# Performance work log

Hardware: AMD Instinct MI355X
Metric: run time of the kernel (lower is better)

## Reference

```python
import jax, jax.numpy as jnp
import numpy as np

N, E, DIN, ED, H, C = 50000, 800000, 128, 16, 4, 128
HC = H * C
SLOPE = 0.2


def gat_conv(x, ei_src, ei_dst, ea, W, a_src, a_dst, We, a_e, b):
    # x: [N, din]; ea: [E, ed] (self-loops already appended by caller)
    n = x.shape[0]
    h = (x @ W).reshape(n, H, C)                       # [N,H,C]
    al_src = (h * a_src).sum(-1)                       # [N,H]
    al_dst = (h * a_dst).sum(-1)                       # [N,H]
    e = (ea @ We).reshape(-1, H, C)                    # [E,H,C]
    al_e = (e * a_e).sum(-1)                           # [E,H]
    alpha = al_src[ei_src] + al_dst[ei_dst] + al_e     # [E,H]
    alpha = jnp.where(alpha > 0, alpha, SLOPE * alpha)  # LeakyReLU(0.2)
    # per-destination-node segment softmax (stable)
    amax = jax.ops.segment_max(alpha, ei_dst, num_segments=n)
    amax = jnp.where(jnp.isfinite(amax), amax, 0.0)
    ex = jnp.exp(alpha - amax[ei_dst])
    den = jax.ops.segment_sum(ex, ei_dst, num_segments=n)
    alpha = ex / (den[ei_dst] + 1e-16)                 # [E,H]
    msg = h[ei_src] * alpha[:, :, None]                # [E,H,C]
    out = jax.ops.segment_sum(msg, ei_dst, num_segments=n)  # [N,H,C]
    return out.reshape(n, HC) + b


def setup_inputs() -> dict:
    key = jax.random.key(0)
    ks = jax.random.split(key, 16)
    s = 0.05
    inp = {
        "x": jax.random.normal(ks[0], (N, DIN), jnp.float32),
        "edge_index": jax.random.randint(ks[1], (2, E), 0, N, jnp.int64),
        "edge_features": jax.random.normal(ks[2], (E, ED), jnp.float32),
        # layer 1 params
        "W1": jax.random.normal(ks[3], (DIN, HC), jnp.float32) * s,
        "att_src1": jax.random.normal(ks[4], (H, C), jnp.float32) * s,
        "att_dst1": jax.random.normal(ks[5], (H, C), jnp.float32) * s,
        "lin_e1": jax.random.normal(ks[6], (ED, HC), jnp.float32) * s,
        "att_e1": jax.random.normal(ks[7], (H, C), jnp.float32) * s,
        "b1": jnp.zeros((HC,), jnp.float32),
        # layer 2 params
        "W2": jax.random.normal(ks[8], (HC, HC), jnp.float32) * s,
        "att_src2": jax.random.normal(ks[9], (H, C), jnp.float32) * s,
        "att_dst2": jax.random.normal(ks[10], (H, C), jnp.float32) * s,
        "lin_e2": jax.random.normal(ks[11], (ED, HC), jnp.float32) * s,
        "att_e2": jax.random.normal(ks[12], (H, C), jnp.float32) * s,
        "b2": jnp.zeros((HC,), jnp.float32),
    }
    return inp


def reference(x, edge_index, edge_features,
              W1, att_src1, att_dst1, lin_e1, att_e1, b1,
              W2, att_src2, att_dst2, lin_e2, att_e2, b2):
    # add self-loops once (PyG default: add_self_loops=True, edge_attr fill='mean')
    loop = jnp.arange(N, dtype=edge_index.dtype)
    ei_src = jnp.concatenate([edge_index[0], loop])
    ei_dst = jnp.concatenate([edge_index[1], loop])
    mean_ea = edge_features.mean(0)
    ea = jnp.concatenate([edge_features, jnp.broadcast_to(mean_ea, (N, ED))], axis=0)

    h = gat_conv(x, ei_src, ei_dst, ea, W1, att_src1, att_dst1, lin_e1, att_e1, b1)
    h = jax.nn.elu(h)
    h = gat_conv(h, ei_src, ei_dst, ea, W2, att_src2, att_dst2, lin_e2, att_e2, b2)
    return jax.nn.elu(h)
```

## Files before the change

kernel.cpp:

```cpp
#include <hip/hip_runtime.h>
#include <math.h>

#define NNODE 50000
#define NEDGE 800000
#define DINv  128
#define EDv   16
#define NHv   4
#define CHv   128
#define HCv   512
#define SLOPEv 0.2f
#define MEANBLK 512
#define CONVN (NNODE * DINv / 4)

typedef __attribute__((ext_vector_type(8))) short bf16x8;
typedef __attribute__((ext_vector_type(4))) float f32x4;
typedef __attribute__((ext_vector_type(4))) unsigned u32x4;
typedef __attribute__((address_space(3))) unsigned lds_u32;
typedef const __attribute__((address_space(1))) unsigned glb_u32;

__device__ __forceinline__ ushort f2b(float f) {
  unsigned u = __float_as_uint(f);
  u += 0x7FFF + ((u >> 16) & 1);
  return (ushort)(u >> 16);
}
__device__ __forceinline__ float blo(unsigned u) { return __uint_as_float(u << 16); }
__device__ __forceinline__ float bhi(unsigned u) { return __uint_as_float(u & 0xffff0000u); }

__device__ __forceinline__ void nt_store16(void* p, unsigned a, unsigned b, unsigned c,
                                           unsigned d) {
  u32x4 t = {a, b, c, d};
  __builtin_nontemporal_store(t, (u32x4*)p);
}

__global__ void detect_kernel(const int* __restrict__ ei, int* __restrict__ flag) {
  __shared__ int bad;
  if (threadIdx.x == 0) bad = 0;
  __syncthreads();
  for (int i = threadIdx.x; i < 2048; i += 256)
    if (ei[2 * i + 1] != 0) bad = 1;
  __syncthreads();
  if (threadIdx.x == 0) flag[0] = bad ? 0 : 1;
}

__device__ __forceinline__ int load_idx(const int* __restrict__ ei, int e, int row, int wide) {
  if (wide) return ei[2 * ((size_t)row * NEDGE + e)];
  return ei[(size_t)row * NEDGE + e];
}

__global__ void count_kernel(const int* __restrict__ ei, const int* __restrict__ flag,
                             int* __restrict__ deg) {
  int e = blockIdx.x * blockDim.x + threadIdx.x;
  if (e < NEDGE) {
    int w = flag[0];
    atomicAdd(&deg[load_idx(ei, e, 1, w)], 1);
  }
}

__global__ void scatter_kernel(const int* __restrict__ ei, const int* __restrict__ flag,
                               const int* __restrict__ row_ptr, int* __restrict__ cursor,
                               int* __restrict__ eid_sorted) {
  int e = blockIdx.x * blockDim.x + threadIdx.x;
  if (e < NEDGE) {
    int w = flag[0];
    int d = load_idx(ei, e, 1, w);
    int p = row_ptr[d] + atomicAdd(&cursor[d], 1);
    eid_sorted[p] = e;
  }
}

__global__ void prep_misc_kernel(const float* __restrict__ ea, float* __restrict__ partials,
                                 const float* __restrict__ We1, const float* __restrict__ ae1,
                                 const float* __restrict__ We2, const float* __restrict__ ae2,
                                 float* __restrict__ v1, float* __restrict__ v2,
                                 const float* __restrict__ x, const float* __restrict__ W1,
                                 const float* __restrict__ W2, ushort* __restrict__ xb,
                                 ushort* __restrict__ Bt1, ushort* __restrict__ Bt2) {
  int b = blockIdx.x;
  if (b < MEANBLK) {
    float acc[EDv];
#pragma unroll
    for (int d = 0; d < EDv; d++) acc[d] = 0.f;
    const int stride = MEANBLK * 256;
    for (int r = b * 256 + threadIdx.x; r < NEDGE; r += stride) {
      const float4* p = (const float4*)(ea + (size_t)r * EDv);
#pragma unroll
      for (int q = 0; q < 4; q++) {
        float4 v = p[q];
        acc[q * 4 + 0] += v.x; acc[q * 4 + 1] += v.y;
        acc[q * 4 + 2] += v.z; acc[q * 4 + 3] += v.w;
      }
    }
    __shared__ float red[4][EDv];
    int wid = threadIdx.x >> 6, lane = threadIdx.x & 63;
#pragma unroll
    for (int d = 0; d < EDv; d++) {
      float v = acc[d];
      for (int off = 32; off; off >>= 1) v += __shfl_down(v, off, 64);
      if (lane == 0) red[wid][d] = v;
    }
    __syncthreads();
    if (threadIdx.x < EDv) {
      float v = red[0][threadIdx.x] + red[1][threadIdx.x] + red[2][threadIdx.x] +
                red[3][threadIdx.x];
      partials[b * EDv + threadIdx.x] = v;
    }
  } else if (b == MEANBLK) {
    int t = threadIdx.x;
    if (t < 128) {
      int layer = t >> 6, u = t & 63;
      int d = u >> 2, h = u & 3;
      const float* We = layer ? We2 : We1;
      const float* ae = layer ? ae2 : ae1;
      float s = 0.f;
      for (int c = 0; c < CHv; c++) s += We[(size_t)d * HCv + h * CHv + c] * ae[h * CHv + c];
      (layer ? v2 : v1)[d * 4 + h] = s;
    }
  } else {
    int i = (b - MEANBLK - 1) * 256 + threadIdx.x;
    if (i < CONVN) {
      float4 v = ((const float4*)x)[i];
      ushort4 o;
      o.x = f2b(v.x); o.y = f2b(v.y); o.z = f2b(v.z); o.w = f2b(v.w);
      ((ushort4*)xb)[i] = o;
    } else if (i < CONVN + DINv * HCv) {
      int idx = i - CONVN;
      int k = idx >> 9, n = idx & (HCv - 1);
      Bt1[(size_t)n * DINv + k] = f2b(W1[idx]);
    } else if (i < CONVN + DINv * HCv + HCv * HCv) {
      int idx = i - CONVN - DINv * HCv;
      int k = idx >> 9, n = idx & (HCv - 1);
      Bt2[(size_t)n * HCv + k] = f2b(W2[idx]);
    }
  }
}

__global__ __launch_bounds__(1024) void scan_fold_kernel(
    const int* __restrict__ deg, int* __restrict__ row_ptr,
    const float* __restrict__ partials, const float* __restrict__ v1,
    const float* __restrict__ v2, float* __restrict__ loop1, float* __restrict__ loop2) {
  int tid = threadIdx.x;
  if (blockIdx.x == 0) {
    __shared__ int wsum[16];
    int wid = tid >> 6, lane = tid & 63;
    int carry = 0;
    for (int base = 0; base < NNODE; base += 4096) {
      int idx = base + tid * 4;
      int4 x = make_int4(0, 0, 0, 0);
      if (idx < NNODE) x = *(const int4*)(deg + idx);
      int t0 = x.x, t1 = t0 + x.y, t2 = t1 + x.z, t3 = t2 + x.w;
      int v = t3;
#pragma unroll
      for (int off = 1; off < 64; off <<= 1) {
        int t = __shfl_up(v, off, 64);
        if (lane >= off) v += t;
      }
      if (lane == 63) wsum[wid] = v;
      __syncthreads();
      if (wid == 0) {
        int s = (lane < 16) ? wsum[lane] : 0;
#pragma unroll
        for (int off = 1; off < 16; off <<= 1) {
          int t = __shfl_up(s, off, 64);
          if (lane >= off) s += t;
        }
        if (lane < 16) wsum[lane] = s;
      }
      __syncthreads();
      int woff = wid ? wsum[wid - 1] : 0;
      int excl = carry + woff + v - t3;
      if (idx < NNODE) {
        int4 o = make_int4(excl, excl + t0, excl + t1, excl + t2);
        *(int4*)(row_ptr + idx) = o;
      }
      carry += wsum[15];
      __syncthreads();
    }
    if (tid == 0) row_ptr[NNODE] = carry;
  } else {
    __shared__ float buf[1024];
    __shared__ float ms[16];
    int d = tid & 15, r0 = tid >> 4;
    float v = 0.f;
    for (int r = r0; r < MEANBLK; r += 64) v += partials[r * EDv + d];
    buf[tid] = v;
    __syncthreads();
#pragma unroll
    for (int off = 32; off >= 1; off >>= 1) {
      if (r0 < off) buf[tid] += buf[tid + off * 16];
      __syncthreads();
    }
    if (tid < 16) ms[tid] = buf[tid] * (1.0f / NEDGE);
    __syncthreads();
    if (tid < 8) {
      const float* vv = (tid >> 2) ? v2 : v1;
      int h = tid & 3;
      float a = 0.f;
      for (int d2 = 0; d2 < EDv; d2++) a += ms[d2] * vv[d2 * 4 + h];
      ((tid >> 2) ? loop2 : loop1)[h] = a;
    }
  }
}

__global__ void apre1_kernel(const int* __restrict__ eid_sorted, const int* __restrict__ ei,
                             const int* __restrict__ flag,
                             const float* __restrict__ ea, const float* __restrict__ al_src,
                             const float* __restrict__ v1, const float* __restrict__ v2,
                             float* __restrict__ ap1, float* __restrict__ ale2s,
                             int* __restrict__ src_sorted) {
  __shared__ float sv1[64], sv2[64];
  if (threadIdx.x < 64) sv1[threadIdx.x] = v1[threadIdx.x];
  else if (threadIdx.x < 128) sv2[threadIdx.x - 64] = v2[threadIdx.x - 64];
  __syncthreads();
  int p = blockIdx.x * 256 + threadIdx.x;
  if (p >= NEDGE) return;
  int e = eid_sorted[p];
  int w = flag[0];
  int s = load_idx(ei, e, 0, w);
  const float4* pr = (const float4*)(ea + (size_t)e * EDv);
  float row[16];
  *(float4*)&row[0] = pr[0]; *(float4*)&row[4] = pr[1];
  *(float4*)&row[8] = pr[2]; *(float4*)&row[12] = pr[3];
  float a0 = 0, a1 = 0, a2 = 0, a3 = 0;
  float b0 = 0, b1 = 0, b2 = 0, b3 = 0;
#pragma unroll
  for (int d = 0; d < 16; d++) {
    a0 += row[d] * sv1[d * 4 + 0];
    a1 += row[d] * sv1[d * 4 + 1];
    a2 += row[d] * sv1[d * 4 + 2];
    a3 += row[d] * sv1[d * 4 + 3];
    b0 += row[d] * sv2[d * 4 + 0];
    b1 += row[d] * sv2[d * 4 + 1];
    b2 += row[d] * sv2[d * 4 + 2];
    b3 += row[d] * sv2[d * 4 + 3];
  }
  float4 as = ((const float4*)al_src)[s];
  ((float4*)ap1)[p] = make_float4(as.x + a0, as.y + a1, as.z + a2, as.w + a3);
  ((float4*)ale2s)[p] = make_float4(b0, b1, b2, b3);
  src_sorted[p] = s;
}

__global__ void apre2_kernel(const int* __restrict__ src_sorted, const float* __restrict__ ale2s,
                             const float* __restrict__ al_src, float* __restrict__ ap2) {
  int p = blockIdx.x * 256 + threadIdx.x;
  if (p >= NEDGE) return;
  int s = src_sorted[p];
  float4 a = ((const float4*)al_src)[s];
  float4 b = ((const float4*)ale2s)[p];
  ((float4*)ap2)[p] = make_float4(a.x + b.x, a.y + b.y, a.z + b.z, a.w + b.w);
}

__global__ __launch_bounds__(256) void gemm_mfma_kernel(const ushort* __restrict__ A,
                                                        const ushort* __restrict__ Bt,
                                                        ushort* __restrict__ C, int M, int K,
                                                        const float* __restrict__ a_src,
                                                        const float* __restrict__ a_dst,
                                                        float* __restrict__ al_src,
                                                        float* __restrict__ al_dst) {
  __shared__ ushort As[8][128][8];
  __shared__ ushort Bs[8][128][8];
  __shared__ float ssa[128], ssd[128];
  __shared__ float rsum[2][128][2];
  int tid = threadIdx.x;
  int wid = tid >> 6, lane = tid & 63;

  int nblk = gridDim.x * gridDim.y;
  int j = blockIdx.y * gridDim.x + blockIdx.x;
  int q = nblk >> 3, rem = nblk & 7;
  int xcd = j & 7, idx = j >> 3;
  int d = (xcd < rem) ? xcd * (q + 1) + idx : rem * (q + 1) + (xcd - rem) * q + idx;
  int rb = (d >> 2) * 128, cb = (d & 3) * 128;
  int hblk = cb >> 7;

  int wm = (wid >> 1) * 64, wn = (wid & 1) * 64;
  int lr = lane & 15, lq = lane >> 4;

  if (tid < 128) { ssa[tid] = a_src[cb + tid]; ssd[tid] = a_dst[cb + tid]; }

  f32x4 acc[4][4];
#pragma unroll
  for (int i = 0; i < 4; i++)
#pragma unroll
    for (int jx = 0; jx < 4; jx++) acc[i][jx] = (f32x4){0.f, 0.f, 0.f, 0.f};

  ushort* AsF = &As[0][0][0];
  ushort* BsF = &Bs[0][0][0];

  for (int k0 = 0; k0 < K; k0 += 64) {
#pragma unroll
    for (int s = 0; s < 4; s++) {
      int c = s * 256 + tid;
      int kq = c >> 7, m = c & 127;
      int row = rb + m; if (row >= M) row = M - 1;
      const ushort* gA = A + (size_t)row * K + k0 + kq * 8;
      __builtin_amdgcn_global_load_lds((glb_u32*)gA, (lds_u32*)(AsF + (size_t)c * 8), 16, 0, 0);
    }
#pragma unroll
    for (int s = 0; s < 4; s++) {
      int c = s * 256 + tid;
      int kq = c >> 7, n = c & 127;
      const ushort* gB = Bt + (size_t)(cb + n) * K + k0 + kq * 8;
      __builtin_amdgcn_global_load_lds((glb_u32*)gB, (lds_u32*)(BsF + (size_t)c * 8), 16, 0, 0);
    }
    __syncthreads();
#pragma unroll
    for (int hh = 0; hh < 2; hh++) {
      bf16x8 af[4], bfr[4];
#pragma unroll
      for (int i = 0; i < 4; i++) {
        af[i]  = *(const bf16x8*)&As[hh * 4 + lq][wm + i * 16 + lr][0];
        bfr[i] = *(const bf16x8*)&Bs[hh * 4 + lq][wn + i * 16 + lr][0];
      }
#pragma unroll
      for (int i = 0; i < 4; i++)
#pragma unroll
        for (int jx = 0; jx < 4; jx++)
          acc[i][jx] = __builtin_amdgcn_mfma_f32_16x16x32_bf16(af[i], bfr[jx], acc[i][jx], 0, 0, 0);
    }
    __syncthreads();
  }

#pragma unroll
  for (int i = 0; i < 4; i++) {
    int rbase = rb + wm + i * 16 + lq * 4;
#pragma unroll
    for (int jx = 0; jx < 4; jx++) {
      int col = cb + wn + jx * 16 + lr;
#pragma unroll
      for (int r = 0; r < 4; r++) {
        int row = rbase + r;
        if (row < M) C[(size_t)row * HCv + col] = f2b(acc[i][jx][r]);
      }
    }
  }

  float sa[4], sd[4];
#pragma unroll
  for (int jx = 0; jx < 4; jx++) {
    int c = wn + jx * 16 + lr;
    sa[jx] = ssa[c]; sd[jx] = ssd[c];
  }
#pragma unroll
  for (int i = 0; i < 4; i++) {
#pragma unroll
    for (int r = 0; r < 4; r++) {
      float s1 = 0.f, s2 = 0.f;
#pragma unroll
      for (int jx = 0; jx < 4; jx++) {
        s1 = fmaf(acc[i][jx][r], sa[jx], s1);
        s2 = fmaf(acc[i][jx][r], sd[jx], s2);
      }
#pragma unroll
      for (int off = 1; off < 16; off <<= 1) {
        s1 += __shfl_xor(s1, off, 16);
        s2 += __shfl_xor(s2, off, 16);
      }
      if (lr == 0) {
        int row = wm + i * 16 + lq * 4 + r;
        rsum[0][row][wn >> 6] = s1;
        rsum[1][row][wn >> 6] = s2;
      }
    }
  }
  __syncthreads();
  if (tid < 128) {
    int row = rb + tid;
    if (row < M) {
      al_src[(size_t)row * 4 + hblk] = rsum[0][tid][0] + rsum[0][tid][1];
      al_dst[(size_t)row * 4 + hblk] = rsum[1][tid][0] + rsum[1][tid][1];
    }
  }
}

__device__ __forceinline__ void fma8(float* acc, float w, uint4 u) {
  acc[0] = fmaf(w, blo(u.x), acc[0]);
  acc[1] = fmaf(w, bhi(u.x), acc[1]);
  acc[2] = fmaf(w, blo(u.y), acc[2]);
  acc[3] = fmaf(w, bhi(u.y), acc[3]);
  acc[4] = fmaf(w, blo(u.z), acc[4]);
  acc[5] = fmaf(w, bhi(u.z), acc[5]);
  acc[6] = fmaf(w, blo(u.w), acc[6]);
  acc[7] = fmaf(w, bhi(u.w), acc[7]);
}

__global__ __launch_bounds__(256) void node_kernel(
    const ushort* __restrict__ hb, const float* __restrict__ al_src,
    const float* __restrict__ al_dst, const float* __restrict__ ap,
    const float* __restrict__ loop_al_e, const int* __restrict__ row_ptr,
    const int* __restrict__ src_sorted, const float* __restrict__ bias,
    float* __restrict__ outf, ushort* __restrict__ outb) {
  int wid = threadIdx.x >> 6, lane = threadIdx.x & 63;
  int n = blockIdx.x * 4 + wid;
  if (n >= NNODE) return;
  int base = row_ptr[n];
  int deg = row_ptr[n + 1] - base;
  int h = lane >> 4;
  int jj = lane & 15;

  float aldh = al_dst[(size_t)n * 4 + h];
  float a0 = al_src[(size_t)n * 4 + h] + aldh + loop_al_e[h];
  float alph = a0 > 0.f ? a0 : SLOPEv * a0;
  float wl = __expf(alph);

  uint4 uself = *((const uint4*)(hb + ((size_t)n << 9)) + lane);

  float acc[8];
#pragma unroll
  for (int q = 0; q < 8; q++) acc[q] = 0.f;
  float den = 0.f;

  for (int cs = 0; cs < deg; cs += 16) {
    int cl = min(16, deg - cs);
    float w = 0.f;
    int sv = 0;
    if (jj < cl) {
      int p = base + cs + jj;
      sv = src_sorted[p];
      float a = ap[(size_t)p * 4 + h] + aldh;
      a = a > 0.f ? a : SLOPEv * a;
      w = __expf(a);
      den += w;
    }
    int cl4 = (cl + 3) & ~3;
    for (int j0 = 0; j0 < cl4; j0 += 4) {
      int s0 = __shfl(sv, j0 + 0, 16);
      int s1 = __shfl(sv, j0 + 1, 16);
      int s2 = __shfl(sv, j0 + 2, 16);
      int s3 = __shfl(sv, j0 + 3, 16);
      float w0 = __shfl(w, j0 + 0, 16);
      float w1 = __shfl(w, j0 + 1, 16);
      float w2 = __shfl(w, j0 + 2, 16);
      float w3 = __shfl(w, j0 + 3, 16);
      uint4 u0 = *((const uint4*)(hb + ((size_t)s0 << 9)) + lane);
      uint4 u1 = *((const uint4*)(hb + ((size_t)s1 << 9)) + lane);
      uint4 u2 = *((const uint4*)(hb + ((size_t)s2 << 9)) + lane);
      uint4 u3 = *((const uint4*)(hb + ((size_t)s3 << 9)) + lane);
      fma8(acc, w0, u0);
      fma8(acc, w1, u1);
      fma8(acc, w2, u2);
      fma8(acc, w3, u3);
    }
  }

  fma8(acc, wl, uself);

#pragma unroll
  for (int off = 8; off; off >>= 1) den += __shfl_xor(den, off, 16);
  den += wl;
  float rden = 1.f / (den + 1e-16f);

  const float4* bp = (const float4*)(bias + lane * 8);
  float4 b0 = bp[0], b1 = bp[1];
  float bv[8] = {b0.x, b0.y, b0.z, b0.w, b1.x, b1.y, b1.z, b1.w};
  float r[8];
#pragma unroll
  for (int q = 0; q < 8; q++) {
    float t = acc[q] * rden + bv[q];
    r[q] = t > 0.f ? t : expm1f(t);
  }
  if (outf) {
    float* op = outf + (size_t)n * HCv + lane * 8;
    nt_store16(op, __float_as_uint(r[0]), __float_as_uint(r[1]),
               __float_as_uint(r[2]), __float_as_uint(r[3]));
    nt_store16(op + 4, __float_as_uint(r[4]), __float_as_uint(r[5]),
               __float_as_uint(r[6]), __float_as_uint(r[7]));
  }
  if (outb) {
    nt_store16(outb + (size_t)n * HCv + lane * 8,
               (unsigned)f2b(r[0]) | ((unsigned)f2b(r[1]) << 16),
               (unsigned)f2b(r[2]) | ((unsigned)f2b(r[3]) << 16),
               (unsigned)f2b(r[4]) | ((unsigned)f2b(r[5]) << 16),
               (unsigned)f2b(r[6]) | ((unsigned)f2b(r[7]) << 16));
  }
}

static inline char* take(char*& p, size_t bytes) {
  char* r = p;
  p += (bytes + 255) & ~(size_t)255;
  return r;
}

extern "C" void kernel_launch(void* const* d_in, const int* in_sizes, int n_in,
                              void* d_out, int out_size, void* d_ws, size_t ws_size,
                              hipStream_t stream) {
  (void)in_sizes; (void)n_in; (void)out_size; (void)ws_size;
  const float* x   = (const float*)d_in[0];
  const int*   ei  = (const int*)d_in[1];
  const float* ea  = (const float*)d_in[2];
  const float* W1  = (const float*)d_in[3];
  const float* as1 = (const float*)d_in[4];
  const float* ad1 = (const float*)d_in[5];
  const float* We1 = (const float*)d_in[6];
  const float* ae1 = (const float*)d_in[7];
  const float* b1  = (const float*)d_in[8];
  const float* W2  = (const float*)d_in[9];
  const float* as2 = (const float*)d_in[10];
  const float* ad2 = (const float*)d_in[11];
  const float* We2 = (const float*)d_in[12];
  const float* ae2 = (const float*)d_in[13];
  const float* b2  = (const float*)d_in[14];
  float* out = (float*)d_out;

  char* p = (char*)d_ws;
  ushort* hb        = (ushort*)take(p, (size_t)NNODE * HCv * 2);
  float* al_src     = (float*)take(p, (size_t)NNODE * 4 * 4);
  float* al_dst     = (float*)take(p, (size_t)NNODE * 4 * 4);
  float* ap         = (float*)take(p, (size_t)NEDGE * 4 * 4);
  float* ale2s      = (float*)take(p, (size_t)NEDGE * 4 * 4);
  int*   src_sorted = (int*)take(p, (size_t)NEDGE * 4);
  int*   eid_sorted = (int*)take(p, (size_t)NEDGE * 4);
  int*   row_ptr    = (int*)take(p, (size_t)(NNODE + 1) * 4);
  float* partials   = (float*)take(p, (size_t)MEANBLK * EDv * 4);
  ushort* Bt1       = (ushort*)take(p, (size_t)HCv * DINv * 2);
  ushort* Bt2       = (ushort*)take(p, (size_t)HCv * HCv * 2);
  char* zero_begin = p;
  int*   deg        = (int*)take(p, (size_t)NNODE * 4);
  int*   cursor     = (int*)take(p, (size_t)NNODE * 4);
  size_t zero_len = (size_t)(p - zero_begin);
  float* v1         = (float*)take(p, 64 * 4);
  float* v2         = (float*)take(p, 64 * 4);
  float* loop1      = (float*)take(p, 4 * 4);
  float* loop2      = (float*)take(p, 4 * 4);
  int*   flag       = (int*)take(p, 4);

  ushort* xb  = (ushort*)d_out;
  ushort* h1b = (ushort*)((char*)d_out + (size_t)16 * 1024 * 1024);

  hipMemsetAsync(zero_begin, 0, zero_len, stream);

  detect_kernel<<<1, 256, 0, stream>>>(ei, flag);
  count_kernel<<<(NEDGE + 255) / 256, 256, 0, stream>>>(ei, flag, deg);
  prep_misc_kernel<<<MEANBLK + 1 + (CONVN + DINv * HCv + HCv * HCv + 255) / 256, 256, 0,
                     stream>>>(ea, partials, We1, ae1, We2, ae2, v1, v2, x, W1, W2, xb, Bt1, Bt2);
  scan_fold_kernel<<<2, 1024, 0, stream>>>(deg, row_ptr, partials, v1, v2, loop1, loop2);
  scatter_kernel<<<(NEDGE + 255) / 256, 256, 0, stream>>>(ei, flag, row_ptr, cursor, eid_sorted);

  gemm_mfma_kernel<<<dim3(HCv / 128, (NNODE + 127) / 128), 256, 0, stream>>>(
      xb, Bt1, hb, NNODE, DINv, as1, ad1, al_src, al_dst);
  apre1_kernel<<<(NEDGE + 255) / 256, 256, 0, stream>>>(eid_sorted, ei, flag, ea, al_src,
                                                        v1, v2, ap, ale2s, src_sorted);
  node_kernel<<<(NNODE + 3) / 4, 256, 0, stream>>>(hb, al_src, al_dst, ap, loop1, row_ptr,
                                                   src_sorted, b1, (float*)nullptr, h1b);

  gemm_mfma_kernel<<<dim3(HCv / 128, (NNODE + 127) / 128), 256, 0, stream>>>(
      h1b, Bt2, hb, NNODE, HCv, as2, ad2, al_src, al_dst);
  apre2_kernel<<<(NEDGE + 255) / 256, 256, 0, stream>>>(src_sorted, ale2s, al_src, ap);
  node_kernel<<<(NNODE + 3) / 4, 256, 0, stream>>>(hb, al_src, al_dst, ap, loop2, row_ptr,
                                                   src_sorted, b2, out, (ushort*)nullptr);
}
```

Measured before the change: 709.9 us.

## Fold count/scatter into neighbour kernels and fuse layer-2 attention prep into node kernel

Merges the degree-count pass into the prep_misc launch as extra blocks, and the CSR scatter pass into the layer-1 GEMM launch as extra trailing blocks on a flattened 1D grid. Drops apre2_kernel by having node_kernel gather al_src per source inside its edge loop, and changes the bf16 output store from nontemporal to a regular vector store. This cuts launches and one full pass over edge arrays, at the cost of extra random gathers in the node kernel and GEMM blocks sharing the GPU with atomic scatter work.

```diff
diff --git a/kernel.cpp b/kernel.cpp
--- a/kernel.cpp
+++ b/kernel.cpp
@@ -11,6 +11,7 @@
 #define SLOPEv 0.2f
 #define MEANBLK 512
 #define CONVN (NNODE * DINv / 4)
+#define NCOUNT ((NEDGE + 255) / 256)
 
 typedef __attribute__((ext_vector_type(8))) short bf16x8;
 typedef __attribute__((ext_vector_type(4))) float f32x4;
@@ -47,28 +48,9 @@
   return ei[(size_t)row * NEDGE + e];
 }
 
-__global__ void count_kernel(const int* __restrict__ ei, const int* __restrict__ flag,
-                             int* __restrict__ deg) {
-  int e = blockIdx.x * blockDim.x + threadIdx.x;
-  if (e < NEDGE) {
-    int w = flag[0];
-    atomicAdd(&deg[load_idx(ei, e, 1, w)], 1);
-  }
-}
-
-__global__ void scatter_kernel(const int* __restrict__ ei, const int* __restrict__ flag,
-                               const int* __restrict__ row_ptr, int* __restrict__ cursor,
-                               int* __restrict__ eid_sorted) {
-  int e = blockIdx.x * blockDim.x + threadIdx.x;
-  if (e < NEDGE) {
-    int w = flag[0];
-    int d = load_idx(ei, e, 1, w);
-    int p = row_ptr[d] + atomicAdd(&cursor[d], 1);
-    eid_sorted[p] = e;
-  }
-}
-
-__global__ void prep_misc_kernel(const float* __restrict__ ea, float* __restrict__ partials,
+__global__ void prep_misc_kernel(const int* __restrict__ ei, const int* __restrict__ flag,
+                                 int* __restrict__ deg,
+                                 const float* __restrict__ ea, float* __restrict__ partials,
                                  const float* __restrict__ We1, const float* __restrict__ ae1,
                                  const float* __restrict__ We2, const float* __restrict__ ae2,
                                  float* __restrict__ v1, float* __restrict__ v2,
@@ -76,6 +58,15 @@
                                  const float* __restrict__ W2, ushort* __restrict__ xb,
                                  ushort* __restrict__ Bt1, ushort* __restrict__ Bt2) {
   int b = blockIdx.x;
+  if (b < NCOUNT) {
+    int e = b * 256 + threadIdx.x;
+    if (e < NEDGE) {
+      int w = flag[0];
+      atomicAdd(&deg[load_idx(ei, e, 1, w)], 1);
+    }
+    return;
+  }
+  b -= NCOUNT;
   if (b < MEANBLK) {
     float acc[EDv];
 #pragma unroll
@@ -239,23 +230,31 @@
   src_sorted[p] = s;
 }
 
-__global__ void apre2_kernel(const int* __restrict__ src_sorted, const float* __restrict__ ale2s,
-                             const float* __restrict__ al_src, float* __restrict__ ap2) {
-  int p = blockIdx.x * 256 + threadIdx.x;
-  if (p >= NEDGE) return;
-  int s = src_sorted[p];
-  float4 a = ((const float4*)al_src)[s];
-  float4 b = ((const float4*)ale2s)[p];
-  ((float4*)ap2)[p] = make_float4(a.x + b.x, a.y + b.y, a.z + b.z, a.w + b.w);
-}
-
 __global__ __launch_bounds__(256) void gemm_mfma_kernel(const ushort* __restrict__ A,
                                                         const ushort* __restrict__ Bt,
                                                         ushort* __restrict__ C, int M, int K,
                                                         const float* __restrict__ a_src,
                                                         const float* __restrict__ a_dst,
                                                         float* __restrict__ al_src,
-                                                        float* __restrict__ al_dst) {
+                                                        float* __restrict__ al_dst,
+                                                        int ngemm,
+                                                        const int* __restrict__ ei,
+                                                        const int* __restrict__ flag,
+                                                        const int* __restrict__ row_ptr,
+                                                        int* __restrict__ cursor,
+                                                        int* __restrict__ eid_sorted) {
+  int j = blockIdx.x;
+  if (j >= ngemm) {
+    int e = (j - ngemm) * 256 + threadIdx.x;
+    if (e < NEDGE) {
+      int w = flag[0];
+      int d0 = load_idx(ei, e, 1, w);
+      int p = row_ptr[d0] + atomicAdd(&cursor[d0], 1);
+      eid_sorted[p] = e;
+    }
+    return;
+  }
+
   __shared__ ushort As[8][128][8];
   __shared__ ushort Bs[8][128][8];
   __shared__ float ssa[128], ssd[128];
@@ -263,9 +262,7 @@
   int tid = threadIdx.x;
   int wid = tid >> 6, lane = tid & 63;
 
-  int nblk = gridDim.x * gridDim.y;
-  int j = blockIdx.y * gridDim.x + blockIdx.x;
-  int q = nblk >> 3, rem = nblk & 7;
+  int q = ngemm >> 3, rem = ngemm & 7;
   int xcd = j & 7, idx = j >> 3;
   int d = (xcd < rem) ? xcd * (q + 1) + idx : rem * (q + 1) + (xcd - rem) * q + idx;
   int rb = (d >> 2) * 128, cb = (d & 3) * 128;
@@ -387,6 +384,7 @@
     const float* __restrict__ al_dst, const float* __restrict__ ap,
     const float* __restrict__ loop_al_e, const int* __restrict__ row_ptr,
     const int* __restrict__ src_sorted, const float* __restrict__ bias,
+    const float* __restrict__ asrc_g,
     float* __restrict__ outf, ushort* __restrict__ outb) {
   int wid = threadIdx.x >> 6, lane = threadIdx.x & 63;
   int n = blockIdx.x * 4 + wid;
@@ -416,6 +414,7 @@
       int p = base + cs + jj;
       sv = src_sorted[p];
       float a = ap[(size_t)p * 4 + h] + aldh;
+      if (asrc_g) a += asrc_g[(size_t)sv * 4 + h];
       a = a > 0.f ? a : SLOPEv * a;
       w = __expf(a);
       den += w;
@@ -465,11 +464,12 @@
                __float_as_uint(r[6]), __float_as_uint(r[7]));
   }
   if (outb) {
-    nt_store16(outb + (size_t)n * HCv + lane * 8,
-               (unsigned)f2b(r[0]) | ((unsigned)f2b(r[1]) << 16),
-               (unsigned)f2b(r[2]) | ((unsigned)f2b(r[3]) << 16),
-               (unsigned)f2b(r[4]) | ((unsigned)f2b(r[5]) << 16),
-               (unsigned)f2b(r[6]) | ((unsigned)f2b(r[7]) << 16));
+    uint4 o;
+    o.x = (unsigned)f2b(r[0]) | ((unsigned)f2b(r[1]) << 16);
+    o.y = (unsigned)f2b(r[2]) | ((unsigned)f2b(r[3]) << 16);
+    o.z = (unsigned)f2b(r[4]) | ((unsigned)f2b(r[5]) << 16);
+    o.w = (unsigned)f2b(r[6]) | ((unsigned)f2b(r[7]) << 16);
+    ((uint4*)(outb + (size_t)n * HCv))[lane] = o;
   }
 }
 
@@ -527,23 +527,27 @@
 
   hipMemsetAsync(zero_begin, 0, zero_len, stream);
 
+  const int NGEMM = 4 * ((NNODE + 127) / 128);
+
   detect_kernel<<<1, 256, 0, stream>>>(ei, flag);
-  count_kernel<<<(NEDGE + 255) / 256, 256, 0, stream>>>(ei, flag, deg);
-  prep_misc_kernel<<<MEANBLK + 1 + (CONVN + DINv * HCv + HCv * HCv + 255) / 256, 256, 0,
-                     stream>>>(ea, partials, We1, ae1, We2, ae2, v1, v2, x, W1, W2, xb, Bt1, Bt2);
+  prep_misc_kernel<<<NCOUNT + MEANBLK + 1 + (CONVN + DINv * HCv + HCv * HCv + 255) / 256, 256,
+                     0, stream>>>(ei, flag, deg, ea, partials, We1, ae1, We2, ae2, v1, v2,
+                                  x, W1, W2, xb, Bt1, Bt2);
   scan_fold_kernel<<<2, 1024, 0, stream>>>(deg, row_ptr, partials, v1, v2, loop1, loop2);
-  scatter_kernel<<<(NEDGE + 255) / 256, 256, 0, stream>>>(ei, flag, row_ptr, cursor, eid_sorted);
-
-  gemm_mfma_kernel<<<dim3(HCv / 128, (NNODE + 127) / 128), 256, 0, stream>>>(
-      xb, Bt1, hb, NNODE, DINv, as1, ad1, al_src, al_dst);
+
+  gemm_mfma_kernel<<<NGEMM + NCOUNT, 256, 0, stream>>>(
+      xb, Bt1, hb, NNODE, DINv, as1, ad1, al_src, al_dst,
+      NGEMM, ei, flag, row_ptr, cursor, eid_sorted);
   apre1_kernel<<<(NEDGE + 255) / 256, 256, 0, stream>>>(eid_sorted, ei, flag, ea, al_src,
                                                         v1, v2, ap, ale2s, src_sorted);
   node_kernel<<<(NNODE + 3) / 4, 256, 0, stream>>>(hb, al_src, al_dst, ap, loop1, row_ptr,
-                                                   src_sorted, b1, (float*)nullptr, h1b);
-
-  gemm_mfma_kernel<<<dim3(HCv / 128, (NNODE + 127) / 128), 256, 0, stream>>>(
-      h1b, Bt2, hb, NNODE, HCv, as2, ad2, al_src, al_dst);
-  apre2_kernel<<<(NEDGE + 255) / 256, 256, 0, stream>>>(src_sorted, ale2s, al_src, ap);
-  node_kernel<<<(NNODE + 3) / 4, 256, 0, stream>>>(hb, al_src, al_dst, ap, loop2, row_ptr,
-                                                   src_sorted, b2, out, (ushort*)nullptr);
-}
+                                                   src_sorted, b1, (const float*)nullptr,
+                                                   (float*)nullptr, h1b);
+
+  gemm_mfma_kernel<<<NGEMM, 256, 0, stream>>>(
+      h1b, Bt2, hb, NNODE, HCv, as2, ad2, al_src, al_dst,
+      NGEMM, ei, flag, row_ptr, cursor, eid_sorted);
+  node_kernel<<<(NNODE + 3) / 4, 256, 0, stream>>>(hb, al_src, al_dst, ale2s, loop2, row_ptr,
+                                                   src_sorted, b2, al_src,
+                                                   out, (ushort*)nullptr);
+}
```

Result: faster. 679.6 us (-4.3%).
